# Kernel optimization log

Hardware: AMD Instinct MI355X
Metric: run time of the kernel (lower is better)

The kernel has to match this reference:

```python
import jax, jax.numpy as jnp
import numpy as np

B, L, K = 4096, 4096, 10


def _sparsemax(z):
    # z: [..., n]; Martins & Astudillo sparsemax along last dim
    n = z.shape[-1]
    zs = -jnp.sort(-z, axis=-1)                      # descending
    cum = jnp.cumsum(zs, axis=-1)
    r = jnp.arange(1, n + 1, dtype=z.dtype)
    support = (1.0 + r * zs) > cum                   # [..., n]
    ksel = jnp.sum(support, axis=-1, keepdims=True)  # support size
    tau = (jnp.take_along_axis(cum, ksel - 1, axis=-1) - 1.0) / ksel.astype(z.dtype)
    return jnp.maximum(z - tau, 0.0)


def _topk_bitvectors(logits, k):
    # k highest-scoring binary vectors z in {0,1}^L under <z, logits>
    # (faithful to the CPU batched_topk: detached logits)
    lg = jax.lax.stop_gradient(logits)
    b, latent = lg.shape
    base = (lg > 0).astype(lg.dtype)                 # argmax config [B, L]
    costs = jnp.abs(lg)                              # flip costs
    neg_small, pos = jax.lax.top_k(-costs, k)        # k smallest costs + positions
    c_small = -neg_small                             # [B, k]
    m = 1 << k                                       # 2^k candidate flip subsets
    bits = ((jnp.arange(m)[:, None] >> jnp.arange(k)[None, :]) & 1).astype(lg.dtype)  # [2^k, k]
    sums = jnp.einsum('mk,bk->bm', bits, c_small)    # total flip cost per subset
    _, best = jax.lax.top_k(-sums, k)                # k cheapest subsets [B, k]
    flips = bits[best]                               # [B, k, k] which small-cost bits to flip
    base_at = jnp.take_along_axis(base, pos, axis=1) # base bit value at flip positions [B, k]
    delta = flips * (1.0 - 2.0 * base_at[:, None, :])  # +1 or -1 where flipped
    bv = jnp.broadcast_to(base[:, None, :], (b, k, latent))
    bidx = jnp.arange(b)[:, None, None]
    cidx = jnp.arange(k)[None, :, None]
    jpos = pos[:, None, :]                           # [B, 1, k]
    bv = bv.at[bidx, cidx, jpos].add(delta)          # scatter flips -> [B, k, L]
    return bv


def reference(logits, k):
    bv = _topk_bitvectors(logits, k)                         # [B, k, L]
    scores = jnp.einsum('bkj,bj->bk', bv, logits)            # [B, k]
    distr = _sparsemax(scores)                               # [B, k]
    p = distr.reshape(-1)
    safe_p = jnp.where(p > 0, p, 1.0)
    entropy = -jnp.sum(jnp.where(p > 0, p * jnp.log(safe_p), 0.0))
    batch_size = logits.shape[0]
    return bv, distr, entropy / batch_size


def setup_inputs() -> dict:
    key = jax.random.key(0)
    logits = jax.random.normal(key, (B, L), dtype=jnp.float32)
    return {"logits": logits, "k": K}
```

## Files before the change

### kernel.cpp

```cpp
#include <hip/hip_runtime.h>
#include <stdint.h>

#define NB   4096
#define LDIM 4096
#define KK   10
#define TPB  256
#define CAP  1024

typedef float fx4 __attribute__((ext_vector_type(4)));

__device__ __forceinline__ unsigned long long wave_min_u64(unsigned long long v) {
#pragma unroll
    for (int off = 1; off < 64; off <<= 1) {
        const unsigned long long o = __shfl_xor(v, off, 64);
        if (o < v) v = o;
    }
    return v;
}

__global__ __launch_bounds__(TPB) void topk_sparsemax(
    const float* __restrict__ logits,
    float* __restrict__ bv,
    float* __restrict__ distr,
    float* __restrict__ entws,
    const int entmode)
{
    __shared__ float s_wsum[4];
    __shared__ int   s_pos[KK];
    __shared__ int   s_sign[KK];
    __shared__ int   s_bestm[KK];
    __shared__ int   s_cnt;
    __shared__ unsigned long long s_cand[CAP];

    const int b    = blockIdx.x;
    const int t    = threadIdx.x;
    const int lane = t & 63;
    const int wv   = t >> 6;
    const float* __restrict__ row = logits + (size_t)b * LDIM;

    float vals[16];
#pragma unroll
    for (int q = 0; q < 4; q++) {
        const float4 f = *(const float4*)(row + (q << 10) + (t << 2));
        vals[q*4+0] = f.x; vals[q*4+1] = f.y; vals[q*4+2] = f.z; vals[q*4+3] = f.w;
    }

    float s0 = 0.f;
#pragma unroll
    for (int i = 0; i < 16; i++) s0 += vals[i] > 0.f ? vals[i] : 0.f;
#pragma unroll
    for (int off = 1; off < 64; off <<= 1) s0 += __shfl_xor(s0, off, 64);
    if (lane == 0) s_wsum[wv] = s0;

    float T = 0.02f;
    int cnt = 0;
    for (int attempt = 0; attempt < 15; attempt++) {
        if (t == 0) s_cnt = 0;
        __syncthreads();
#pragma unroll
        for (int i = 0; i < 16; i++) {
            const float v    = vals[i];
            const float cost = fabsf(v);
            if (cost < T) {
                const int idx = ((i >> 2) << 10) + (t << 2) + (i & 3);
                const unsigned long long pk =
                    ((unsigned long long)__float_as_uint(cost) << 32)
                    | (unsigned)((idx << 1) | (v > 0.f ? 1 : 0));
                const int p = atomicAdd(&s_cnt, 1);
                if (p < CAP) s_cand[p] = pk;
            }
        }
        __syncthreads();
        cnt = s_cnt;
        if (cnt >= KK && cnt <= CAP) break;
        T = (cnt < KK) ? T * 4.0f : T * 0.25f;
        __syncthreads();
    }

    if (wv == 0) {
        const float S0 = (s_wsum[0] + s_wsum[1]) + (s_wsum[2] + s_wsum[3]);
        float csm[KK];
        unsigned long long prev = 0ull;

        if (cnt >= KK && cnt <= CAP) {
            const int nc = cnt;
#pragma unroll
            for (int c = 0; c < KK; c++) {
                unsigned long long best = ~0ull;
                for (int p = lane; p < nc; p += 64) {
                    const unsigned long long pk = s_cand[p];
                    if ((c == 0 || pk > prev) && pk < best) best = pk;
                }
                best = wave_min_u64(best);
                prev = best;
                csm[c] = __uint_as_float((unsigned)(best >> 32));
                if (lane == 0) {
                    const unsigned lo = (unsigned)best;
                    s_pos[c]  = (int)(lo >> 1);
                    s_sign[c] = (int)(lo & 1u);
                }
            }
        } else {
#pragma unroll
            for (int c = 0; c < KK; c++) {
                unsigned long long best = ~0ull;
                for (int p = lane; p < LDIM; p += 64) {
                    const float v    = row[p];
                    const float cost = fabsf(v);
                    const unsigned long long pk =
                        ((unsigned long long)__float_as_uint(cost) << 32)
                        | (unsigned)((p << 1) | (v > 0.f ? 1 : 0));
                    if ((c == 0 || pk > prev) && pk < best) best = pk;
                }
                best = wave_min_u64(best);
                prev = best;
                csm[c] = __uint_as_float((unsigned)(best >> 32));
                if (lane == 0) {
                    const unsigned lo = (unsigned)best;
                    s_pos[c]  = (int)(lo >> 1);
                    s_sign[c] = (int)(lo & 1u);
                }
            }
        }

        float sums[16];
#pragma unroll
        for (int i = 0; i < 16; i++) {
            const int m = (lane << 4) | i;
            float acc = 0.f;
#pragma unroll
            for (int j = 0; j < KK; j++) acc += (m & (1 << j)) ? csm[j] : 0.f;
            sums[i] = acc;
        }

        float zc[KK];
        unsigned long long prev2 = 0ull;
#pragma unroll
        for (int c = 0; c < KK; c++) {
            unsigned long long best = ~0ull;
#pragma unroll
            for (int i = 0; i < 16; i++) {
                const unsigned long long pk =
                    ((unsigned long long)__float_as_uint(sums[i]) << 32)
                    | (unsigned)((lane << 4) | i);
                if ((c == 0 || pk > prev2) && pk < best) best = pk;
            }
            best = wave_min_u64(best);
            prev2 = best;
            zc[c] = S0 - __uint_as_float((unsigned)(best >> 32));
            if (lane == 0) s_bestm[c] = (int)((unsigned)best & 1023u);
        }

        if (lane == 0) {
            float acc = 0.f; int ks = 0;
#pragma unroll
            for (int r = 1; r <= KK; r++) {
                acc += zc[r-1];
                if (1.f + (float)r * zc[r-1] > acc) ks++;
            }
            float acc2 = 0.f;
#pragma unroll
            for (int r = 0; r < KK; r++) if (r < ks) acc2 += zc[r];
            const float tau = (acc2 - 1.f) / (float)ks;
            float entl = 0.f;
            float* drow = distr + b * KK;
#pragma unroll
            for (int c = 0; c < KK; c++) {
                float p = zc[c] - tau;
                p = p > 0.f ? p : 0.f;
                drow[c] = p;
                if (p > 0.f) entl -= p * logf(p);
            }
            if (entmode) entws[b] = entl;
            else         atomicAdd(entws, entl * (1.0f / (float)NB));
        }
    }

    __syncthreads();

    unsigned fm[KK];
#pragma unroll
    for (int j = 0; j < KK; j++) {
        unsigned m = 0u;
#pragma unroll
        for (int c = 0; c < KK; c++)
            m |= (((unsigned)s_bestm[c] >> j) & 1u) << c;
        fm[j] = m;
    }
    int posr[KK], sgnr[KK];
#pragma unroll
    for (int j = 0; j < KK; j++) { posr[j] = s_pos[j]; sgnr[j] = s_sign[j]; }

    unsigned rowflip[16]; float flipval[16]; float basef[16];
#pragma unroll
    for (int i = 0; i < 16; i++) {
        const int col = ((i >> 2) << 10) + (t << 2) + (i & 3);
        unsigned rf = 0u; float fv = 0.f;
#pragma unroll
        for (int j = 0; j < KK; j++) {
            if (posr[j] == col) { rf = fm[j]; fv = sgnr[j] ? 0.f : 1.f; }
        }
        rowflip[i] = rf; flipval[i] = fv;
        basef[i]   = vals[i] > 0.f ? 1.f : 0.f;
    }

    float* out0 = bv + (size_t)b * (KK * LDIM);
#pragma unroll
    for (int c = 0; c < KK; c++) {
        float* orow = out0 + c * LDIM + (t << 2);
#pragma unroll
        for (int q = 0; q < 4; q++) {
            fx4 v;
            v.x = ((rowflip[q*4+0] >> c) & 1u) ? flipval[q*4+0] : basef[q*4+0];
            v.y = ((rowflip[q*4+1] >> c) & 1u) ? flipval[q*4+1] : basef[q*4+1];
            v.z = ((rowflip[q*4+2] >> c) & 1u) ? flipval[q*4+2] : basef[q*4+2];
            v.w = ((rowflip[q*4+3] >> c) & 1u) ? flipval[q*4+3] : basef[q*4+3];
            __builtin_nontemporal_store(v, (fx4*)(orow + (q << 10)));
        }
    }
}

__global__ __launch_bounds__(256) void ent_reduce(
    const float* __restrict__ ws, float* __restrict__ ent)
{
    __shared__ float sw[4];
    const int t = threadIdx.x, lane = t & 63, wv = t >> 6;
    float s = 0.f;
    for (int i = t; i < NB; i += 256) s += ws[i];
#pragma unroll
    for (int off = 1; off < 64; off <<= 1) s += __shfl_xor(s, off, 64);
    if (lane == 0) sw[wv] = s;
    __syncthreads();
    if (t == 0) *ent = (sw[0] + sw[1] + sw[2] + sw[3]) * (1.0f / (float)NB);
}

extern "C" void kernel_launch(void* const* d_in, const int* in_sizes, int n_in,
                              void* d_out, int out_size, void* d_ws, size_t ws_size,
                              hipStream_t stream)
{
    const float* logits = (const float*)d_in[0];
    float* out   = (float*)d_out;
    float* bv    = out;
    float* distr = out + (size_t)NB * KK * LDIM;
    float* ent   = distr + (size_t)NB * KK;

    if (ws_size >= (size_t)NB * sizeof(float)) {
        topk_sparsemax<<<dim3(NB), dim3(TPB), 0, stream>>>(
            logits, bv, distr, (float*)d_ws, 1);
        ent_reduce<<<dim3(1), dim3(256), 0, stream>>>((const float*)d_ws, ent);
    } else {
        (void)hipMemsetAsync(ent, 0, sizeof(float), stream);
        topk_sparsemax<<<dim3(NB), dim3(TPB), 0, stream>>>(
            logits, bv, distr, ent, 0);
    }
}
```

Before: 723.6 us.

## Split top-k selection and bitvector writing into separate kernels

The fused per-row kernel becomes two kernels. A selection kernel computes the flip positions, masks, sparsemax and per-row entropy, then writes compact per-row metadata to workspace. A second kernel with four blocks per row re-reads the logits and streams out the bitvector rows. The aim is to stop three idle waves from waiting on wave 0's serial selection before the large output write, and to give the write-bound phase more parallelism. The cost is an extra kernel launch, a second read of the logits, and a metadata round trip through global memory. The old fused path is kept as a fallback when the workspace is too small.

```diff
diff --git a/kernel.cpp b/kernel.cpp
--- a/kernel.cpp
+++ b/kernel.cpp
@@ -18,12 +18,11 @@
     return v;
 }
 
-__global__ __launch_bounds__(TPB) void topk_sparsemax(
+__global__ __launch_bounds__(TPB) void select_rows(
     const float* __restrict__ logits,
-    float* __restrict__ bv,
     float* __restrict__ distr,
-    float* __restrict__ entws,
-    const int entmode)
+    float* __restrict__ entp,
+    unsigned* __restrict__ meta)
 {
     __shared__ float s_wsum[4];
     __shared__ int   s_pos[KK];
@@ -77,11 +76,237 @@
         __syncthreads();
     }
 
+    if (wv != 0) return;
+
+    const float S0 = (s_wsum[0] + s_wsum[1]) + (s_wsum[2] + s_wsum[3]);
+    float csm[KK];
+    unsigned long long prev = 0ull;
+
+    if (cnt >= KK && cnt <= CAP) {
+        const int nc = cnt;
+#pragma unroll
+        for (int c = 0; c < KK; c++) {
+            unsigned long long best = ~0ull;
+            for (int p = lane; p < nc; p += 64) {
+                const unsigned long long pk = s_cand[p];
+                if ((c == 0 || pk > prev) && pk < best) best = pk;
+            }
+            best = wave_min_u64(best);
+            prev = best;
+            csm[c] = __uint_as_float((unsigned)(best >> 32));
+            if (lane == 0) {
+                const unsigned lo = (unsigned)best;
+                s_pos[c]  = (int)(lo >> 1);
+                s_sign[c] = (int)(lo & 1u);
+            }
+        }
+    } else {
+#pragma unroll
+        for (int c = 0; c < KK; c++) {
+            unsigned long long best = ~0ull;
+            for (int p = lane; p < LDIM; p += 64) {
+                const float v    = row[p];
+                const float cost = fabsf(v);
+                const unsigned long long pk =
+                    ((unsigned long long)__float_as_uint(cost) << 32)
+                    | (unsigned)((p << 1) | (v > 0.f ? 1 : 0));
+                if ((c == 0 || pk > prev) && pk < best) best = pk;
+            }
+            best = wave_min_u64(best);
+            prev = best;
+            csm[c] = __uint_as_float((unsigned)(best >> 32));
+            if (lane == 0) {
+                const unsigned lo = (unsigned)best;
+                s_pos[c]  = (int)(lo >> 1);
+                s_sign[c] = (int)(lo & 1u);
+            }
+        }
+    }
+
+    float sums[16];
+#pragma unroll
+    for (int i = 0; i < 16; i++) {
+        const int m = (lane << 4) | i;
+        float acc = 0.f;
+#pragma unroll
+        for (int j = 0; j < KK; j++) acc += (m & (1 << j)) ? csm[j] : 0.f;
+        sums[i] = acc;
+    }
+
+    float zc[KK];
+    unsigned long long prev2 = 0ull;
+#pragma unroll
+    for (int c = 0; c < KK; c++) {
+        unsigned long long best = ~0ull;
+#pragma unroll
+        for (int i = 0; i < 16; i++) {
+            const unsigned long long pk =
+                ((unsigned long long)__float_as_uint(sums[i]) << 32)
+                | (unsigned)((lane << 4) | i);
+            if ((c == 0 || pk > prev2) && pk < best) best = pk;
+        }
+        best = wave_min_u64(best);
+        prev2 = best;
+        zc[c] = S0 - __uint_as_float((unsigned)(best >> 32));
+        if (lane == 0) s_bestm[c] = (int)((unsigned)best & 1023u);
+    }
+
+    if (lane == 0) {
+        float acc = 0.f; int ks = 0;
+#pragma unroll
+        for (int r = 1; r <= KK; r++) {
+            acc += zc[r-1];
+            if (1.f + (float)r * zc[r-1] > acc) ks++;
+        }
+        float acc2 = 0.f;
+#pragma unroll
+        for (int r = 0; r < KK; r++) if (r < ks) acc2 += zc[r];
+        const float tau = (acc2 - 1.f) / (float)ks;
+        float entl = 0.f;
+        float* drow = distr + b * KK;
+#pragma unroll
+        for (int c = 0; c < KK; c++) {
+            float p = zc[c] - tau;
+            p = p > 0.f ? p : 0.f;
+            drow[c] = p;
+            if (p > 0.f) entl -= p * logf(p);
+        }
+        entp[b] = entl;
+
+        unsigned* mrow = meta + b * KK;
+#pragma unroll
+        for (int s = 0; s < KK; s++) {
+            unsigned fm = 0u;
+#pragma unroll
+            for (int c = 0; c < KK; c++)
+                fm |= (((unsigned)s_bestm[c] >> s) & 1u) << c;
+            mrow[s] = (unsigned)s_pos[s] | (fm << 12) | ((unsigned)s_sign[s] << 22);
+        }
+    }
+}
+
+__global__ __launch_bounds__(TPB) void bv_writer(
+    const float* __restrict__ logits,
+    const unsigned* __restrict__ meta,
+    float* __restrict__ bv)
+{
+    __shared__ unsigned s_m[KK];
+    const int bid = blockIdx.x;
+    const int b   = bid >> 2;
+    const int seg = bid & 3;
+    const int t   = threadIdx.x;
+    if (t < KK) s_m[t] = meta[b * KK + t];
+    __syncthreads();
+
+    const int j0 = (seg << 10) + (t << 2);
+    const float4 f = *(const float4*)(logits + (size_t)b * LDIM + j0);
+    float basef[4];
+    basef[0] = f.x > 0.f ? 1.f : 0.f;
+    basef[1] = f.y > 0.f ? 1.f : 0.f;
+    basef[2] = f.z > 0.f ? 1.f : 0.f;
+    basef[3] = f.w > 0.f ? 1.f : 0.f;
+
+    unsigned rf[4] = {0u, 0u, 0u, 0u};
+    float    fv[4] = {0.f, 0.f, 0.f, 0.f};
+#pragma unroll
+    for (int s = 0; s < KK; s++) {
+        const unsigned m   = s_m[s];
+        const int      pos = (int)(m & 0xFFFu);
+        const unsigned msk = (m >> 12) & 0x3FFu;
+        const float    val = ((m >> 22) & 1u) ? 0.f : 1.f;
+#pragma unroll
+        for (int e = 0; e < 4; e++)
+            if (pos == j0 + e) { rf[e] = msk; fv[e] = val; }
+    }
+
+    float* out0 = bv + (size_t)b * (KK * LDIM) + j0;
+#pragma unroll
+    for (int c = 0; c < KK; c++) {
+        fx4 v;
+        v.x = ((rf[0] >> c) & 1u) ? fv[0] : basef[0];
+        v.y = ((rf[1] >> c) & 1u) ? fv[1] : basef[1];
+        v.z = ((rf[2] >> c) & 1u) ? fv[2] : basef[2];
+        v.w = ((rf[3] >> c) & 1u) ? fv[3] : basef[3];
+        __builtin_nontemporal_store(v, (fx4*)(out0 + c * LDIM));
+    }
+}
+
+__global__ __launch_bounds__(256) void ent_reduce(
+    const float* __restrict__ ws, float* __restrict__ ent)
+{
+    __shared__ float sw[4];
+    const int t = threadIdx.x, lane = t & 63, wv = t >> 6;
+    float s = 0.f;
+    for (int i = t; i < NB; i += 256) s += ws[i];
+#pragma unroll
+    for (int off = 1; off < 64; off <<= 1) s += __shfl_xor(s, off, 64);
+    if (lane == 0) sw[wv] = s;
+    __syncthreads();
+    if (t == 0) *ent = (sw[0] + sw[1] + sw[2] + sw[3]) * (1.0f / (float)NB);
+}
+
+__global__ __launch_bounds__(TPB) void topk_sparsemax_fused(
+    const float* __restrict__ logits,
+    float* __restrict__ bv,
+    float* __restrict__ distr,
+    float* __restrict__ ent)
+{
+    __shared__ float s_wsum[4];
+    __shared__ int   s_pos[KK];
+    __shared__ int   s_sign[KK];
+    __shared__ int   s_bestm[KK];
+    __shared__ int   s_cnt;
+    __shared__ unsigned long long s_cand[CAP];
+
+    const int b    = blockIdx.x;
+    const int t    = threadIdx.x;
+    const int lane = t & 63;
+    const int wv   = t >> 6;
+    const float* __restrict__ row = logits + (size_t)b * LDIM;
+
+    float vals[16];
+#pragma unroll
+    for (int q = 0; q < 4; q++) {
+        const float4 f = *(const float4*)(row + (q << 10) + (t << 2));
+        vals[q*4+0] = f.x; vals[q*4+1] = f.y; vals[q*4+2] = f.z; vals[q*4+3] = f.w;
+    }
+
+    float s0 = 0.f;
+#pragma unroll
+    for (int i = 0; i < 16; i++) s0 += vals[i] > 0.f ? vals[i] : 0.f;
+#pragma unroll
+    for (int off = 1; off < 64; off <<= 1) s0 += __shfl_xor(s0, off, 64);
+    if (lane == 0) s_wsum[wv] = s0;
+
+    float T = 0.02f;
+    int cnt = 0;
+    for (int attempt = 0; attempt < 15; attempt++) {
+        if (t == 0) s_cnt = 0;
+        __syncthreads();
+#pragma unroll
+        for (int i = 0; i < 16; i++) {
+            const float v    = vals[i];
+            const float cost = fabsf(v);
+            if (cost < T) {
+                const int idx = ((i >> 2) << 10) + (t << 2) + (i & 3);
+                const unsigned long long pk =
+                    ((unsigned long long)__float_as_uint(cost) << 32)
+                    | (unsigned)((idx << 1) | (v > 0.f ? 1 : 0));
+                const int p = atomicAdd(&s_cnt, 1);
+                if (p < CAP) s_cand[p] = pk;
+            }
+        }
+        __syncthreads();
+        cnt = s_cnt;
+        if (cnt >= KK && cnt <= CAP) break;
+        T = (cnt < KK) ? T * 4.0f : T * 0.25f;
+        __syncthreads();
+    }
+
     if (wv == 0) {
         const float S0 = (s_wsum[0] + s_wsum[1]) + (s_wsum[2] + s_wsum[3]);
         float csm[KK];
         unsigned long long prev = 0ull;
-
         if (cnt >= KK && cnt <= CAP) {
             const int nc = cnt;
 #pragma unroll
@@ -122,7 +347,6 @@
                 }
             }
         }
-
         float sums[16];
 #pragma unroll
         for (int i = 0; i < 16; i++) {
@@ -132,7 +356,6 @@
             for (int j = 0; j < KK; j++) acc += (m & (1 << j)) ? csm[j] : 0.f;
             sums[i] = acc;
         }
-
         float zc[KK];
         unsigned long long prev2 = 0ull;
 #pragma unroll
@@ -150,7 +373,6 @@
             zc[c] = S0 - __uint_as_float((unsigned)(best >> 32));
             if (lane == 0) s_bestm[c] = (int)((unsigned)best & 1023u);
         }
-
         if (lane == 0) {
             float acc = 0.f; int ks = 0;
 #pragma unroll
@@ -171,8 +393,7 @@
                 drow[c] = p;
                 if (p > 0.f) entl -= p * logf(p);
             }
-            if (entmode) entws[b] = entl;
-            else         atomicAdd(entws, entl * (1.0f / (float)NB));
+            atomicAdd(ent, entl * (1.0f / (float)NB));
         }
     }
 
@@ -195,12 +416,12 @@
 #pragma unroll
     for (int i = 0; i < 16; i++) {
         const int col = ((i >> 2) << 10) + (t << 2) + (i & 3);
-        unsigned rf = 0u; float fv = 0.f;
+        unsigned rfm = 0u; float fvv = 0.f;
 #pragma unroll
         for (int j = 0; j < KK; j++) {
-            if (posr[j] == col) { rf = fm[j]; fv = sgnr[j] ? 0.f : 1.f; }
-        }
-        rowflip[i] = rf; flipval[i] = fv;
+            if (posr[j] == col) { rfm = fm[j]; fvv = sgnr[j] ? 0.f : 1.f; }
+        }
+        rowflip[i] = rfm; flipval[i] = fvv;
         basef[i]   = vals[i] > 0.f ? 1.f : 0.f;
     }
 
@@ -218,20 +439,6 @@
             __builtin_nontemporal_store(v, (fx4*)(orow + (q << 10)));
         }
     }
-}
-
-__global__ __launch_bounds__(256) void ent_reduce(
-    const float* __restrict__ ws, float* __restrict__ ent)
-{
-    __shared__ float sw[4];
-    const int t = threadIdx.x, lane = t & 63, wv = t >> 6;
-    float s = 0.f;
-    for (int i = t; i < NB; i += 256) s += ws[i];
-#pragma unroll
-    for (int off = 1; off < 64; off <<= 1) s += __shfl_xor(s, off, 64);
-    if (lane == 0) sw[wv] = s;
-    __syncthreads();
-    if (t == 0) *ent = (sw[0] + sw[1] + sw[2] + sw[3]) * (1.0f / (float)NB);
 }
 
 extern "C" void kernel_launch(void* const* d_in, const int* in_sizes, int n_in,
@@ -244,13 +451,16 @@
     float* distr = out + (size_t)NB * KK * LDIM;
     float* ent   = distr + (size_t)NB * KK;
 
-    if (ws_size >= (size_t)NB * sizeof(float)) {
-        topk_sparsemax<<<dim3(NB), dim3(TPB), 0, stream>>>(
-            logits, bv, distr, (float*)d_ws, 1);
-        ent_reduce<<<dim3(1), dim3(256), 0, stream>>>((const float*)d_ws, ent);
+    const size_t need = (size_t)NB * sizeof(float)
+                      + (size_t)NB * KK * sizeof(unsigned);
+    if (ws_size >= need) {
+        float*    entp = (float*)d_ws;
+        unsigned* meta = (unsigned*)((float*)d_ws + NB);
+        select_rows<<<dim3(NB), dim3(TPB), 0, stream>>>(logits, distr, entp, meta);
+        bv_writer <<<dim3(NB * 4), dim3(TPB), 0, stream>>>(logits, meta, bv);
+        ent_reduce<<<dim3(1), dim3(256), 0, stream>>>(entp, ent);
     } else {
         (void)hipMemsetAsync(ent, 0, sizeof(float), stream);
-        topk_sparsemax<<<dim3(NB), dim3(TPB), 0, stream>>>(
-            logits, bv, distr, ent, 0);
-    }
-}
+        topk_sparsemax_fused<<<dim3(NB), dim3(TPB), 0, stream>>>(logits, bv, distr, ent);
+    }
+}
```

New measurement: 701.1 us. 3.1% less time.
